# Kernel optimization log

Hardware: AMD Instinct MI355X
Metric: run time of the kernel (lower is better)

## Reference

```python
import jax, jax.numpy as jnp
import numpy as np

D_MODEL = 64
N_HEAD = 8
MAX_REL = 16  # module hardcodes max_relative_position = 16
B, S = 8, 1024


def _linear_params(k, fan_in, fan_out):
    kw, kb = jax.random.split(k)
    s = 1.0 / np.sqrt(fan_in)
    W = jax.random.uniform(kw, (fan_in, fan_out), jnp.float32, -s, s)
    b = jax.random.uniform(kb, (fan_out,), jnp.float32, -s, s)
    return W, b


def setup_inputs() -> dict:
    key = jax.random.key(0)
    ks = jax.random.split(key, 10)
    Wq, bq = _linear_params(ks[0], D_MODEL, D_MODEL * N_HEAD)
    Wk, bk = _linear_params(ks[1], D_MODEL, D_MODEL * N_HEAD)
    Wv, bv = _linear_params(ks[2], D_MODEL, D_MODEL * N_HEAD)
    Wo, bo = _linear_params(ks[3], D_MODEL * N_HEAD, D_MODEL)
    Wkr, bkr = _linear_params(ks[4], D_MODEL, D_MODEL)
    Wqr, bqr = _linear_params(ks[5], D_MODEL, D_MODEL)
    p = jax.random.normal(ks[6], (2 * MAX_REL + 1, D_MODEL), jnp.float32)
    query = jax.random.normal(ks[7], (B, S, D_MODEL), jnp.float32)
    key_t = jax.random.normal(ks[8], (B, S, D_MODEL), jnp.float32)
    value = jax.random.normal(ks[9], (B, S, D_MODEL), jnp.float32)
    return dict(query=query, key=key_t, value=value,
                Wq=Wq, bq=bq, Wk=Wk, bk=bk, Wv=Wv, bv=bv,
                Wo=Wo, bo=bo, Wkr=Wkr, bkr=bkr, Wqr=Wqr, bqr=bqr, p=p)


def reference(query, key, value, Wq, bq, Wk, bk, Wv, bv, Wo, bo, Wkr, bkr, Wqr, bqr, p):
    Bsz, Sq, d = query.shape
    H = Wq.shape[1] // d  # head_dim == d_model in this module
    scale = jnp.sqrt(jnp.asarray(3 * d, jnp.float32))

    def heads(x, W, b):
        return (x @ W + b).reshape(Bsz, -1, H, d).transpose(0, 2, 1, 3)  # [B,H,S,d]

    q1 = heads(query, Wq, bq)
    k1 = heads(key, Wk, bk)
    v1 = heads(value, Wv, bv)

    # content-content term
    attn1 = jnp.einsum('bhqd,bhkd->bhqk', q1, k1)

    # relative-position terms. make_table uses clamp(dist, min=16, max=16)+16,
    # so every gather index is exactly 2*MAX_REL -> the gathered value is the
    # single column 2*MAX_REL of each table, broadcast over the last axis.
    k_r = p @ Wkr + bkr  # [2*MAX_REL+1, d]
    q_r = p @ Wqr + bqr
    attn2 = jnp.einsum('bhqd,d->bhq', q1, k_r[2 * MAX_REL])[..., None]  # [B,H,Sq,1]
    attn3 = jnp.einsum('bhkd,d->bhk', k1, q_r[2 * MAX_REL])[..., None]  # [B,H,Sk,1] (Sk==Sq)

    attn = jax.nn.softmax((attn1 + attn2 + attn3) / scale, axis=-1)
    x = jnp.einsum('bhqk,bhkd->bhqd', attn, v1)
    x = x.transpose(0, 2, 1, 3).reshape(Bsz, Sq, H * d)
    return x @ Wo + bo
```

## Files before the change

### kernel.cpp

```cpp
#include <hip/hip_runtime.h>
#include <hip/hip_bf16.h>


#define N_HEAD 8
#define BATCH  8
#define SEQ    1024
#define DMH    512
#define SC2    0.10411804386480816f

typedef __hip_bfloat16 bf16;
typedef __bf16 bf16x8 __attribute__((ext_vector_type(8)));
typedef __bf16 bf16x4 __attribute__((ext_vector_type(4)));
typedef float  f32x4  __attribute__((ext_vector_type(4)));

__global__ __launch_bounds__(256)
void init_kernel(const float* __restrict__ Wq, const float* __restrict__ Wk,
                 const float* __restrict__ Wv, const float* __restrict__ Wo,
                 const float* __restrict__ bo, float* __restrict__ out,
                 bf16* __restrict__ WqT, bf16* __restrict__ WkT,
                 bf16* __restrict__ WvT, bf16* __restrict__ WoT)
{
    const int idx = blockIdx.x * 256 + threadIdx.x;
    out[idx] = bo[idx & 63];
    if (idx < 512 * 64) {
        {
            const int n = idx >> 6, k = idx & 63;
            WqT[idx] = __float2bfloat16(Wq[(size_t)k * 512 + n]);
            WkT[idx] = __float2bfloat16(Wk[(size_t)k * 512 + n]);
            WvT[idx] = __float2bfloat16(Wv[(size_t)k * 512 + n]);
        }
        {
            const int c = idx >> 9, k = idx & 511;
            WoT[idx] = __float2bfloat16(Wo[(size_t)k * 64 + c]);
        }
    }
}

__global__ __launch_bounds__(256)
void qkv_mfma_kernel(const float* __restrict__ Xq, const float* __restrict__ Xk,
                     const float* __restrict__ Xv,
                     const bf16* __restrict__ WqT, const bf16* __restrict__ WkT,
                     const bf16* __restrict__ WvT,
                     const float* __restrict__ bq, const float* __restrict__ bk,
                     const float* __restrict__ bv,
                     bf16* __restrict__ Qh, bf16* __restrict__ Kh,
                     bf16* __restrict__ Vt)
{
    const int rt    = blockIdx.x;
    const int ct    = blockIdx.y;
    const int which = blockIdx.z;

    const float* __restrict__ X    = which == 0 ? Xq  : (which == 1 ? Xk  : Xv);
    const bf16*  __restrict__ WT   = which == 0 ? WqT : (which == 1 ? WkT : WvT);
    const float* __restrict__ bias = which == 0 ? bq  : (which == 1 ? bk  : bv);

    __shared__ __align__(16) bf16 Xs [128 * 72];
    __shared__ __align__(16) bf16 Wts[64 * 72];
    __shared__ float Bs[64];

    const int tid  = threadIdx.x;
    const int w4   = tid >> 6;
    const int lane = tid & 63;
    const int t16  = lane & 15;
    const int quad = lane >> 4;

    if (tid < 64) Bs[tid] = bias[ct * 64 + tid];
    for (int i = tid; i < 2048; i += 256) {
        const int r = i >> 4, c4 = (i & 15) << 2;
        const float4 v = *(const float4*)&X[(size_t)(rt * 128 + r) * 64 + c4];
        bf16 t[4] = {__float2bfloat16(v.x), __float2bfloat16(v.y),
                     __float2bfloat16(v.z), __float2bfloat16(v.w)};
        *(bf16x4*)&Xs[r * 72 + c4] = *(bf16x4*)t;
    }
    for (int i = tid; i < 512; i += 256) {
        const int r8 = i >> 3, c8 = (i & 7) << 3;
        *(bf16x8*)&Wts[r8 * 72 + c8] = *(const bf16x8*)&WT[(size_t)(ct * 64 + r8) * 64 + c8];
    }
    __syncthreads();

    bf16x8 bf0[4], bf1[4];
#pragma unroll
    for (int nt = 0; nt < 4; nt++) {
        bf0[nt] = *(const bf16x8*)&Wts[(nt * 16 + t16) * 72 + 0  + quad * 8];
        bf1[nt] = *(const bf16x8*)&Wts[(nt * 16 + t16) * 72 + 32 + quad * 8];
    }

    f32x4 acc[2][4];
#pragma unroll
    for (int rs = 0; rs < 2; rs++) {
        const int m = rs * 64 + w4 * 16 + t16;
        const bf16x8 af0 = *(const bf16x8*)&Xs[m * 72 + 0  + quad * 8];
        const bf16x8 af1 = *(const bf16x8*)&Xs[m * 72 + 32 + quad * 8];
#pragma unroll
        for (int nt = 0; nt < 4; nt++) {
            acc[rs][nt] = (f32x4){0.f, 0.f, 0.f, 0.f};
            acc[rs][nt] = __builtin_amdgcn_mfma_f32_16x16x32_bf16(af0, bf0[nt], acc[rs][nt], 0, 0, 0);
            acc[rs][nt] = __builtin_amdgcn_mfma_f32_16x16x32_bf16(af1, bf1[nt], acc[rs][nt], 0, 0, 0);
        }
    }

    const int b     = rt >> 3;
    const int sbase = (rt & 7) * 128;

    if (which < 2) {
        bf16* O = which == 0 ? Qh : Kh;
        const float sc = (which == 0) ? SC2 : 1.0f;
#pragma unroll
        for (int rs = 0; rs < 2; rs++)
#pragma unroll
            for (int rr = 0; rr < 4; rr++) {
                const int s = sbase + rs * 64 + w4 * 16 + quad * 4 + rr;
                bf16* dst = O + (((size_t)b * N_HEAD + ct) * SEQ + s) * 64 + t16;
#pragma unroll
                for (int nt = 0; nt < 4; nt++)
                    dst[nt * 16] = __float2bfloat16((acc[rs][nt][rr] + Bs[nt * 16 + t16]) * sc);
            }
    } else {
        __syncthreads();
        bf16* VtS = Xs;
#pragma unroll
        for (int rs = 0; rs < 2; rs++)
#pragma unroll
            for (int nt = 0; nt < 4; nt++)
#pragma unroll
                for (int rr = 0; rr < 4; rr++) {
                    const int rloc = rs * 64 + w4 * 16 + quad * 4 + rr;
                    VtS[(nt * 16 + t16) * 136 + rloc] =
                        __float2bfloat16(acc[rs][nt][rr] + Bs[nt * 16 + t16]);
                }
        __syncthreads();
        for (int i = tid; i < 1024; i += 256) {
            const int c = i >> 4, r8 = (i & 15) << 3;
            *(bf16x8*)&Vt[(((size_t)b * N_HEAD + c) * 0 + ((size_t)b * N_HEAD + ct) * 64 + c) * SEQ + sbase + r8] =
                *(const bf16x8*)&VtS[c * 136 + r8];
        }
    }
}

__global__ __launch_bounds__(512, 4)
void flash_attn_kernel(const bf16* __restrict__ Qh, const bf16* __restrict__ Kh,
                       const bf16* __restrict__ Vt, const bf16* __restrict__ WoT,
                       float* __restrict__ out)
{
    const int bhx  = blockIdx.x;
    const int qt   = blockIdx.y;
    const int b    = bhx >> 3;
    const int h    = bhx & 7;
    const int tid  = threadIdx.x;
    const int wave = tid >> 6;
    const int w4   = wave & 3;
    const int kh   = wave >> 2;
    const int lane = tid & 63;
    const int t16  = lane & 15;
    const int quad = lane >> 4;

    const size_t bh = (size_t)b * N_HEAD + h;
    const bf16* __restrict__ Qp  = Qh + bh * (SEQ * 64);
    const bf16* __restrict__ Kp  = Kh + bh * (SEQ * 64);
    const bf16* __restrict__ Vtp = Vt + bh * (64 * SEQ);

    __shared__ __align__(16) bf16 smem[36864];
    bf16* KsB  = smem;
    bf16* VtsB = smem + 9216;
    bf16* PsB  = smem + 18432;

    bf16x8 qf0[2], qf1[2];
#pragma unroll
    for (int rs = 0; rs < 2; rs++) {
        const int qrow = qt * 128 + rs * 64 + w4 * 16 + t16;
        qf0[rs] = *(const bf16x8*)(Qp + (size_t)qrow * 64 + 0  + quad * 8);
        qf1[rs] = *(const bf16x8*)(Qp + (size_t)qrow * 64 + 32 + quad * 8);
    }

    f32x4 Of[2][4];
    float l_i[2][4];
#pragma unroll
    for (int rs = 0; rs < 2; rs++) {
#pragma unroll
        for (int nt = 0; nt < 4; nt++) Of[rs][nt] = (f32x4){0.f, 0.f, 0.f, 0.f};
#pragma unroll
        for (int rr = 0; rr < 4; rr++) l_i[rs][rr] = 0.f;
    }

    const int r8s = tid >> 3;
    const int c8s = (tid & 7) << 3;
    bf16x8 pre[4];
#define LOAD_TILES(kt_)                                                          \
    do {                                                                         \
        pre[0] = *(const bf16x8*)&Kp [(size_t)((kt_) * 64 + r8s) * 64 + c8s];    \
        pre[1] = *(const bf16x8*)&Vtp[(size_t)r8s * SEQ + (kt_) * 64 + c8s];     \
        pre[2] = *(const bf16x8*)&Kp [(size_t)(512 + (kt_) * 64 + r8s) * 64 + c8s]; \
        pre[3] = *(const bf16x8*)&Vtp[(size_t)r8s * SEQ + 512 + (kt_) * 64 + c8s];  \
    } while (0)

    LOAD_TILES(0);

    for (int kt = 0; kt < 8; kt++) {
        *(bf16x8*)&KsB [       r8s * 72 + c8s] = pre[0];
        *(bf16x8*)&VtsB[       r8s * 72 + c8s] = pre[1];
        *(bf16x8*)&KsB [4608 + r8s * 72 + c8s] = pre[2];
        *(bf16x8*)&VtsB[4608 + r8s * 72 + c8s] = pre[3];
        __syncthreads();

        if (kt < 7) LOAD_TILES(kt + 1);

        const bf16* Ksw  = KsB  + kh * 4608;
        const bf16* Vtsw = VtsB + kh * 4608;

#pragma unroll
        for (int rs = 0; rs < 2; rs++) {
            f32x4 Sf[4];
#pragma unroll
            for (int nt = 0; nt < 4; nt++) {
                Sf[nt] = (f32x4){0.f, 0.f, 0.f, 0.f};
                const bf16x8 kf0 = *(const bf16x8*)&Ksw[(nt * 16 + t16) * 72 + 0  + quad * 8];
                const bf16x8 kf1 = *(const bf16x8*)&Ksw[(nt * 16 + t16) * 72 + 32 + quad * 8];
                Sf[nt] = __builtin_amdgcn_mfma_f32_16x16x32_bf16(qf0[rs], kf0, Sf[nt], 0, 0, 0);
                Sf[nt] = __builtin_amdgcn_mfma_f32_16x16x32_bf16(qf1[rs], kf1, Sf[nt], 0, 0, 0);
            }

#pragma unroll
            for (int nt = 0; nt < 4; nt++)
#pragma unroll
                for (int rr = 0; rr < 4; rr++) {
                    const float p = exp2f(Sf[nt][rr]);
                    Sf[nt][rr] = p;
                    l_i[rs][rr] += p;
                }

            bf16* Psw = PsB + (rs * 8 + wave) * 1152;
#pragma unroll
            for (int nt = 0; nt < 4; nt++)
#pragma unroll
                for (int rr = 0; rr < 4; rr++)
                    Psw[(quad * 4 + rr) * 72 + nt * 16 + t16] =
                        __float2bfloat16(Sf[nt][rr]);

            const bf16x8 pf0 = *(const bf16x8*)&Psw[t16 * 72 + 0  + quad * 8];
            const bf16x8 pf1 = *(const bf16x8*)&Psw[t16 * 72 + 32 + quad * 8];
#pragma unroll
            for (int nt = 0; nt < 4; nt++) {
                const bf16x8 vf0 = *(const bf16x8*)&Vtsw[(nt * 16 + t16) * 72 + 0  + quad * 8];
                const bf16x8 vf1 = *(const bf16x8*)&Vtsw[(nt * 16 + t16) * 72 + 32 + quad * 8];
                Of[rs][nt] = __builtin_amdgcn_mfma_f32_16x16x32_bf16(pf0, vf0, Of[rs][nt], 0, 0, 0);
                Of[rs][nt] = __builtin_amdgcn_mfma_f32_16x16x32_bf16(pf1, vf1, Of[rs][nt], 0, 0, 0);
            }
        }
        __syncthreads();
    }
#undef LOAD_TILES

    float* Xch = (float*)smem;
    float* Lch = (float*)(smem + 17408);
    bf16*  WoS = smem + 22528;
    bf16*  Pe  = smem + 27136;

    if (kh == 1) {
#pragma unroll
        for (int rs = 0; rs < 2; rs++) {
#pragma unroll
            for (int nt = 0; nt < 4; nt++)
#pragma unroll
                for (int rr = 0; rr < 4; rr++)
                    Xch[((w4 * 2 + rs) * 64 + lane) * 17 + nt * 4 + rr] = Of[rs][nt][rr];
#pragma unroll
            for (int rr = 0; rr < 4; rr++)
                Lch[((w4 * 2 + rs) * 64 + lane) * 5 + rr] = l_i[rs][rr];
        }
    }
    {
        const int r8 = tid >> 3, c8 = (tid & 7) << 3;
        *(bf16x8*)&WoS[r8 * 72 + c8] = *(const bf16x8*)&WoT[(size_t)r8 * 512 + h * 64 + c8];
    }
    __syncthreads();

    if (kh == 0) {
#pragma unroll
        for (int rs = 0; rs < 2; rs++) {
#pragma unroll
            for (int nt = 0; nt < 4; nt++)
#pragma unroll
                for (int rr = 0; rr < 4; rr++)
                    Of[rs][nt][rr] += Xch[((w4 * 2 + rs) * 64 + lane) * 17 + nt * 4 + rr];
#pragma unroll
            for (int rr = 0; rr < 4; rr++)
                l_i[rs][rr] += Lch[((w4 * 2 + rs) * 64 + lane) * 5 + rr];
        }

#pragma unroll
        for (int rs = 0; rs < 2; rs++)
#pragma unroll
            for (int off = 8; off >= 1; off >>= 1)
#pragma unroll
                for (int rr = 0; rr < 4; rr++)
                    l_i[rs][rr] += __shfl_xor(l_i[rs][rr], off, 64);

        bf16* Pew = Pe + w4 * 1152;
#pragma unroll
        for (int rs = 0; rs < 2; rs++) {
            float inv_l[4];
#pragma unroll
            for (int rr = 0; rr < 4; rr++) inv_l[rr] = 1.0f / l_i[rs][rr];
#pragma unroll
            for (int nt = 0; nt < 4; nt++)
#pragma unroll
                for (int rr = 0; rr < 4; rr++)
                    Pew[(quad * 4 + rr) * 72 + nt * 16 + t16] =
                        __float2bfloat16(Of[rs][nt][rr] * inv_l[rr]);

            const bf16x8 pf0 = *(const bf16x8*)&Pew[t16 * 72 + 0  + quad * 8];
            const bf16x8 pf1 = *(const bf16x8*)&Pew[t16 * 72 + 32 + quad * 8];

            f32x4 R[4];
#pragma unroll
            for (int nt = 0; nt < 4; nt++) {
                R[nt] = (f32x4){0.f, 0.f, 0.f, 0.f};
                const bf16x8 wf0 = *(const bf16x8*)&WoS[(nt * 16 + t16) * 72 + 0  + quad * 8];
                const bf16x8 wf1 = *(const bf16x8*)&WoS[(nt * 16 + t16) * 72 + 32 + quad * 8];
                R[nt] = __builtin_amdgcn_mfma_f32_16x16x32_bf16(pf0, wf0, R[nt], 0, 0, 0);
                R[nt] = __builtin_amdgcn_mfma_f32_16x16x32_bf16(pf1, wf1, R[nt], 0, 0, 0);
            }

            const int srow_base = qt * 128 + rs * 64 + w4 * 16 + quad * 4;
#pragma unroll
            for (int rr = 0; rr < 4; rr++) {
                const size_t base = ((size_t)b * SEQ + srow_base + rr) * 64;
#pragma unroll
                for (int nt = 0; nt < 4; nt++)
                    atomicAdd(&out[base + nt * 16 + t16], R[nt][rr]);
            }
        }
    }
}

extern "C" void kernel_launch(void* const* d_in, const int* in_sizes, int n_in,
                              void* d_out, int out_size, void* d_ws, size_t ws_size,
                              hipStream_t stream)
{
    const float* query = (const float*)d_in[0];
    const float* key_  = (const float*)d_in[1];
    const float* value = (const float*)d_in[2];
    const float* Wq    = (const float*)d_in[3];
    const float* bq    = (const float*)d_in[4];
    const float* Wk    = (const float*)d_in[5];
    const float* bk    = (const float*)d_in[6];
    const float* Wv    = (const float*)d_in[7];
    const float* bv    = (const float*)d_in[8];
    const float* Wo    = (const float*)d_in[9];
    const float* bo    = (const float*)d_in[10];

    float* out = (float*)d_out;
    char* ws   = (char*)d_ws;
    bf16* Qh  = (bf16*)(ws + (size_t) 0 * 1024 * 1024);
    bf16* Kh  = (bf16*)(ws + (size_t) 8 * 1024 * 1024);
    bf16* Vt  = (bf16*)(ws + (size_t)16 * 1024 * 1024);
    bf16* WoT = (bf16*)(ws + (size_t)24 * 1024 * 1024);
    bf16* WqT = (bf16*)(ws + (size_t)24 * 1024 * 1024 + 65536);
    bf16* WkT = (bf16*)(ws + (size_t)24 * 1024 * 1024 + 131072);
    bf16* WvT = (bf16*)(ws + (size_t)24 * 1024 * 1024 + 196608);

    init_kernel<<<dim3(2048), 256, 0, stream>>>(Wq, Wk, Wv, Wo, bo, out,
                                                WqT, WkT, WvT, WoT);
    qkv_mfma_kernel<<<dim3(64, 8, 3), 256, 0, stream>>>(
        query, key_, value, WqT, WkT, WvT, bq, bk, bv, Qh, Kh, Vt);
    flash_attn_kernel<<<dim3(64, 8), 512, 0, stream>>>(Qh, Kh, Vt, WoT, out);
}
```

Before: 145.1 us.

## Restructure flash attention to load K/V directly from global, per-wave row tiles

The attention kernel drops the shared-memory K/V staging, the double-buffer prefetch and the split-key reduction across wave halves. Each wave now owns 16 query rows over all 1024 keys and reads K and V fragments straight from global memory (relying on cache). The row-sum is computed with an MFMA against a ones vector instead of scalar adds plus shuffles. The grid doubles to 64-row tiles with 256-thread blocks for higher occupancy, at the cost of redundant global and L2 traffic for K/V across the waves of a block. A leftover no-op term in the V-transpose store index is also removed.

```diff
diff --git a/kernel.cpp b/kernel.cpp
--- a/kernel.cpp
+++ b/kernel.cpp
@@ -131,13 +131,13 @@
         __syncthreads();
         for (int i = tid; i < 1024; i += 256) {
             const int c = i >> 4, r8 = (i & 15) << 3;
-            *(bf16x8*)&Vt[(((size_t)b * N_HEAD + c) * 0 + ((size_t)b * N_HEAD + ct) * 64 + c) * SEQ + sbase + r8] =
+            *(bf16x8*)&Vt[(((size_t)b * N_HEAD + ct) * 64 + c) * SEQ + sbase + r8] =
                 *(const bf16x8*)&VtS[c * 136 + r8];
         }
     }
 }
 
-__global__ __launch_bounds__(512, 4)
+__global__ __launch_bounds__(256, 8)
 void flash_attn_kernel(const bf16* __restrict__ Qh, const bf16* __restrict__ Kh,
                        const bf16* __restrict__ Vt, const bf16* __restrict__ WoT,
                        float* __restrict__ out)
@@ -147,9 +147,7 @@
     const int b    = bhx >> 3;
     const int h    = bhx & 7;
     const int tid  = threadIdx.x;
-    const int wave = tid >> 6;
-    const int w4   = wave & 3;
-    const int kh   = wave >> 2;
+    const int w4   = tid >> 6;
     const int lane = tid & 63;
     const int t16  = lane & 15;
     const int quad = lane >> 4;
@@ -159,177 +157,95 @@
     const bf16* __restrict__ Kp  = Kh + bh * (SEQ * 64);
     const bf16* __restrict__ Vtp = Vt + bh * (64 * SEQ);
 
-    __shared__ __align__(16) bf16 smem[36864];
-    bf16* KsB  = smem;
-    bf16* VtsB = smem + 9216;
-    bf16* PsB  = smem + 18432;
-
-    bf16x8 qf0[2], qf1[2];
-#pragma unroll
-    for (int rs = 0; rs < 2; rs++) {
-        const int qrow = qt * 128 + rs * 64 + w4 * 16 + t16;
-        qf0[rs] = *(const bf16x8*)(Qp + (size_t)qrow * 64 + 0  + quad * 8);
-        qf1[rs] = *(const bf16x8*)(Qp + (size_t)qrow * 64 + 32 + quad * 8);
-    }
-
-    f32x4 Of[2][4];
-    float l_i[2][4];
-#pragma unroll
-    for (int rs = 0; rs < 2; rs++) {
-#pragma unroll
-        for (int nt = 0; nt < 4; nt++) Of[rs][nt] = (f32x4){0.f, 0.f, 0.f, 0.f};
-#pragma unroll
-        for (int rr = 0; rr < 4; rr++) l_i[rs][rr] = 0.f;
-    }
-
-    const int r8s = tid >> 3;
-    const int c8s = (tid & 7) << 3;
-    bf16x8 pre[4];
-#define LOAD_TILES(kt_)                                                          \
-    do {                                                                         \
-        pre[0] = *(const bf16x8*)&Kp [(size_t)((kt_) * 64 + r8s) * 64 + c8s];    \
-        pre[1] = *(const bf16x8*)&Vtp[(size_t)r8s * SEQ + (kt_) * 64 + c8s];     \
-        pre[2] = *(const bf16x8*)&Kp [(size_t)(512 + (kt_) * 64 + r8s) * 64 + c8s]; \
-        pre[3] = *(const bf16x8*)&Vtp[(size_t)r8s * SEQ + 512 + (kt_) * 64 + c8s];  \
-    } while (0)
-
-    LOAD_TILES(0);
-
-    for (int kt = 0; kt < 8; kt++) {
-        *(bf16x8*)&KsB [       r8s * 72 + c8s] = pre[0];
-        *(bf16x8*)&VtsB[       r8s * 72 + c8s] = pre[1];
-        *(bf16x8*)&KsB [4608 + r8s * 72 + c8s] = pre[2];
-        *(bf16x8*)&VtsB[4608 + r8s * 72 + c8s] = pre[3];
-        __syncthreads();
-
-        if (kt < 7) LOAD_TILES(kt + 1);
-
-        const bf16* Ksw  = KsB  + kh * 4608;
-        const bf16* Vtsw = VtsB + kh * 4608;
-
-#pragma unroll
-        for (int rs = 0; rs < 2; rs++) {
-            f32x4 Sf[4];
-#pragma unroll
-            for (int nt = 0; nt < 4; nt++) {
-                Sf[nt] = (f32x4){0.f, 0.f, 0.f, 0.f};
-                const bf16x8 kf0 = *(const bf16x8*)&Ksw[(nt * 16 + t16) * 72 + 0  + quad * 8];
-                const bf16x8 kf1 = *(const bf16x8*)&Ksw[(nt * 16 + t16) * 72 + 32 + quad * 8];
-                Sf[nt] = __builtin_amdgcn_mfma_f32_16x16x32_bf16(qf0[rs], kf0, Sf[nt], 0, 0, 0);
-                Sf[nt] = __builtin_amdgcn_mfma_f32_16x16x32_bf16(qf1[rs], kf1, Sf[nt], 0, 0, 0);
-            }
-
-#pragma unroll
-            for (int nt = 0; nt < 4; nt++)
-#pragma unroll
-                for (int rr = 0; rr < 4; rr++) {
-                    const float p = exp2f(Sf[nt][rr]);
-                    Sf[nt][rr] = p;
-                    l_i[rs][rr] += p;
-                }
-
-            bf16* Psw = PsB + (rs * 8 + wave) * 1152;
-#pragma unroll
-            for (int nt = 0; nt < 4; nt++)
-#pragma unroll
-                for (int rr = 0; rr < 4; rr++)
-                    Psw[(quad * 4 + rr) * 72 + nt * 16 + t16] =
-                        __float2bfloat16(Sf[nt][rr]);
-
-            const bf16x8 pf0 = *(const bf16x8*)&Psw[t16 * 72 + 0  + quad * 8];
-            const bf16x8 pf1 = *(const bf16x8*)&Psw[t16 * 72 + 32 + quad * 8];
-#pragma unroll
-            for (int nt = 0; nt < 4; nt++) {
-                const bf16x8 vf0 = *(const bf16x8*)&Vtsw[(nt * 16 + t16) * 72 + 0  + quad * 8];
-                const bf16x8 vf1 = *(const bf16x8*)&Vtsw[(nt * 16 + t16) * 72 + 32 + quad * 8];
-                Of[rs][nt] = __builtin_amdgcn_mfma_f32_16x16x32_bf16(pf0, vf0, Of[rs][nt], 0, 0, 0);
-                Of[rs][nt] = __builtin_amdgcn_mfma_f32_16x16x32_bf16(pf1, vf1, Of[rs][nt], 0, 0, 0);
-            }
-        }
-        __syncthreads();
-    }
-#undef LOAD_TILES
-
-    float* Xch = (float*)smem;
-    float* Lch = (float*)(smem + 17408);
-    bf16*  WoS = smem + 22528;
-    bf16*  Pe  = smem + 27136;
-
-    if (kh == 1) {
-#pragma unroll
-        for (int rs = 0; rs < 2; rs++) {
-#pragma unroll
-            for (int nt = 0; nt < 4; nt++)
-#pragma unroll
-                for (int rr = 0; rr < 4; rr++)
-                    Xch[((w4 * 2 + rs) * 64 + lane) * 17 + nt * 4 + rr] = Of[rs][nt][rr];
+    __shared__ __align__(16) bf16 Ps[4][16 * 72];
+
+    const int qrow = qt * 64 + w4 * 16 + t16;
+    const bf16x8 qf0 = *(const bf16x8*)(Qp + (size_t)qrow * 64 + 0  + quad * 8);
+    const bf16x8 qf1 = *(const bf16x8*)(Qp + (size_t)qrow * 64 + 32 + quad * 8);
+
+    bf16 one_s[8];
+#pragma unroll
+    for (int j = 0; j < 8; j++) one_s[j] = __float2bfloat16(1.0f);
+    const bf16x8 ones = *(const bf16x8*)one_s;
+
+    f32x4 Of[4];
+    f32x4 Lf = (f32x4){0.f, 0.f, 0.f, 0.f};
+#pragma unroll
+    for (int nt = 0; nt < 4; nt++) Of[nt] = (f32x4){0.f, 0.f, 0.f, 0.f};
+
+    bf16* Psw = Ps[w4];
+
+    for (int kt = 0; kt < 16; kt++) {
+        f32x4 Sf[4];
+#pragma unroll
+        for (int nt = 0; nt < 4; nt++) {
+            const size_t kb = (size_t)(kt * 64 + nt * 16 + t16) * 64 + quad * 8;
+            const bf16x8 kf0 = *(const bf16x8*)&Kp[kb + 0];
+            const bf16x8 kf1 = *(const bf16x8*)&Kp[kb + 32];
+            Sf[nt] = (f32x4){0.f, 0.f, 0.f, 0.f};
+            Sf[nt] = __builtin_amdgcn_mfma_f32_16x16x32_bf16(qf0, kf0, Sf[nt], 0, 0, 0);
+            Sf[nt] = __builtin_amdgcn_mfma_f32_16x16x32_bf16(qf1, kf1, Sf[nt], 0, 0, 0);
+        }
+
+#pragma unroll
+        for (int nt = 0; nt < 4; nt++)
 #pragma unroll
             for (int rr = 0; rr < 4; rr++)
-                Lch[((w4 * 2 + rs) * 64 + lane) * 5 + rr] = l_i[rs][rr];
-        }
-    }
-    {
-        const int r8 = tid >> 3, c8 = (tid & 7) << 3;
-        *(bf16x8*)&WoS[r8 * 72 + c8] = *(const bf16x8*)&WoT[(size_t)r8 * 512 + h * 64 + c8];
-    }
-    __syncthreads();
-
-    if (kh == 0) {
-#pragma unroll
-        for (int rs = 0; rs < 2; rs++) {
-#pragma unroll
-            for (int nt = 0; nt < 4; nt++)
-#pragma unroll
-                for (int rr = 0; rr < 4; rr++)
-                    Of[rs][nt][rr] += Xch[((w4 * 2 + rs) * 64 + lane) * 17 + nt * 4 + rr];
+                Sf[nt][rr] = exp2f(Sf[nt][rr]);
+
+#pragma unroll
+        for (int nt = 0; nt < 4; nt++)
 #pragma unroll
             for (int rr = 0; rr < 4; rr++)
-                l_i[rs][rr] += Lch[((w4 * 2 + rs) * 64 + lane) * 5 + rr];
-        }
-
-#pragma unroll
-        for (int rs = 0; rs < 2; rs++)
-#pragma unroll
-            for (int off = 8; off >= 1; off >>= 1)
-#pragma unroll
-                for (int rr = 0; rr < 4; rr++)
-                    l_i[rs][rr] += __shfl_xor(l_i[rs][rr], off, 64);
-
-        bf16* Pew = Pe + w4 * 1152;
-#pragma unroll
-        for (int rs = 0; rs < 2; rs++) {
-            float inv_l[4];
-#pragma unroll
-            for (int rr = 0; rr < 4; rr++) inv_l[rr] = 1.0f / l_i[rs][rr];
-#pragma unroll
-            for (int nt = 0; nt < 4; nt++)
-#pragma unroll
-                for (int rr = 0; rr < 4; rr++)
-                    Pew[(quad * 4 + rr) * 72 + nt * 16 + t16] =
-                        __float2bfloat16(Of[rs][nt][rr] * inv_l[rr]);
-
-            const bf16x8 pf0 = *(const bf16x8*)&Pew[t16 * 72 + 0  + quad * 8];
-            const bf16x8 pf1 = *(const bf16x8*)&Pew[t16 * 72 + 32 + quad * 8];
-
-            f32x4 R[4];
-#pragma unroll
-            for (int nt = 0; nt < 4; nt++) {
-                R[nt] = (f32x4){0.f, 0.f, 0.f, 0.f};
-                const bf16x8 wf0 = *(const bf16x8*)&WoS[(nt * 16 + t16) * 72 + 0  + quad * 8];
-                const bf16x8 wf1 = *(const bf16x8*)&WoS[(nt * 16 + t16) * 72 + 32 + quad * 8];
-                R[nt] = __builtin_amdgcn_mfma_f32_16x16x32_bf16(pf0, wf0, R[nt], 0, 0, 0);
-                R[nt] = __builtin_amdgcn_mfma_f32_16x16x32_bf16(pf1, wf1, R[nt], 0, 0, 0);
-            }
-
-            const int srow_base = qt * 128 + rs * 64 + w4 * 16 + quad * 4;
-#pragma unroll
-            for (int rr = 0; rr < 4; rr++) {
-                const size_t base = ((size_t)b * SEQ + srow_base + rr) * 64;
-#pragma unroll
-                for (int nt = 0; nt < 4; nt++)
-                    atomicAdd(&out[base + nt * 16 + t16], R[nt][rr]);
-            }
-        }
+                Psw[(quad * 4 + rr) * 72 + nt * 16 + t16] = __float2bfloat16(Sf[nt][rr]);
+
+        const bf16x8 pf0 = *(const bf16x8*)&Psw[t16 * 72 + 0  + quad * 8];
+        const bf16x8 pf1 = *(const bf16x8*)&Psw[t16 * 72 + 32 + quad * 8];
+
+        Lf = __builtin_amdgcn_mfma_f32_16x16x32_bf16(pf0, ones, Lf, 0, 0, 0);
+        Lf = __builtin_amdgcn_mfma_f32_16x16x32_bf16(pf1, ones, Lf, 0, 0, 0);
+
+#pragma unroll
+        for (int nt = 0; nt < 4; nt++) {
+            const size_t vb = (size_t)(nt * 16 + t16) * SEQ + kt * 64 + quad * 8;
+            const bf16x8 vf0 = *(const bf16x8*)&Vtp[vb + 0];
+            const bf16x8 vf1 = *(const bf16x8*)&Vtp[vb + 32];
+            Of[nt] = __builtin_amdgcn_mfma_f32_16x16x32_bf16(pf0, vf0, Of[nt], 0, 0, 0);
+            Of[nt] = __builtin_amdgcn_mfma_f32_16x16x32_bf16(pf1, vf1, Of[nt], 0, 0, 0);
+        }
+    }
+
+    float inv_l[4];
+#pragma unroll
+    for (int rr = 0; rr < 4; rr++) inv_l[rr] = 1.0f / Lf[rr];
+#pragma unroll
+    for (int nt = 0; nt < 4; nt++)
+#pragma unroll
+        for (int rr = 0; rr < 4; rr++)
+            Psw[(quad * 4 + rr) * 72 + nt * 16 + t16] =
+                __float2bfloat16(Of[nt][rr] * inv_l[rr]);
+
+    const bf16x8 pf0 = *(const bf16x8*)&Psw[t16 * 72 + 0  + quad * 8];
+    const bf16x8 pf1 = *(const bf16x8*)&Psw[t16 * 72 + 32 + quad * 8];
+
+    f32x4 R[4];
+#pragma unroll
+    for (int nt = 0; nt < 4; nt++) {
+        const size_t wb = (size_t)(nt * 16 + t16) * 512 + h * 64 + quad * 8;
+        const bf16x8 wf0 = *(const bf16x8*)&WoT[wb + 0];
+        const bf16x8 wf1 = *(const bf16x8*)&WoT[wb + 32];
+        R[nt] = (f32x4){0.f, 0.f, 0.f, 0.f};
+        R[nt] = __builtin_amdgcn_mfma_f32_16x16x32_bf16(pf0, wf0, R[nt], 0, 0, 0);
+        R[nt] = __builtin_amdgcn_mfma_f32_16x16x32_bf16(pf1, wf1, R[nt], 0, 0, 0);
+    }
+
+    const int srow_base = qt * 64 + w4 * 16 + quad * 4;
+#pragma unroll
+    for (int rr = 0; rr < 4; rr++) {
+        const size_t base = ((size_t)b * SEQ + srow_base + rr) * 64;
+#pragma unroll
+        for (int nt = 0; nt < 4; nt++)
+            atomicAdd(&out[base + nt * 16 + t16], R[nt][rr]);
     }
 }
 
@@ -363,5 +279,5 @@
                                                 WqT, WkT, WvT, WoT);
     qkv_mfma_kernel<<<dim3(64, 8, 3), 256, 0, stream>>>(
         query, key_, value, WqT, WkT, WvT, bq, bk, bv, Qh, Kh, Vt);
-    flash_attn_kernel<<<dim3(64, 8), 512, 0, stream>>>(Qh, Kh, Vt, WoT, out);
-}
+    flash_attn_kernel<<<dim3(64, 16), 256, 0, stream>>>(Qh, Kh, Vt, WoT, out);
+}
```

Result: slower. 231.3 us (+59.4%).
